# Kernel optimization log

Hardware: AMD Instinct MI355X
Metric: run time of the kernel (lower is better)

The kernel has to match this reference:

```python
import jax, jax.numpy as jnp
import numpy as np

EMBED_DIM = 1024
NUM_HEADS = 16
HEAD_DIM = EMBED_DIM // NUM_HEADS
WINDOW = 64


def apply_rope(x):
    # x: (B, H, S, d), rotate-half RoPE with base 10000
    B, H, S, d = x.shape
    half = d // 2
    pos = jnp.arange(S, dtype=x.dtype)
    freqs = 1.0 / (10000.0 ** (jnp.arange(half, dtype=x.dtype) / half))
    ang = pos[:, None] * freqs[None, :]              # (S, half)
    cos, sin = jnp.cos(ang), jnp.sin(ang)
    x1, x2 = x[..., :half], x[..., half:]
    return jnp.concatenate([x1 * cos - x2 * sin, x1 * sin + x2 * cos], axis=-1)


def setup_inputs() -> dict:
    key = jax.random.key(0)
    ks = jax.random.split(key, 12)
    B, S, D = 1, 2048, EMBED_DIM
    scale = 1.0 / np.sqrt(D)
    inp = {
        'query': jax.random.normal(ks[0], (B, S, D), jnp.float32),
        'key':   jax.random.normal(ks[1], (B, S, D), jnp.float32),
        'value': jax.random.normal(ks[2], (B, S, D), jnp.float32),
        'q_w': jax.random.normal(ks[3], (D, D), jnp.float32) * scale,
        'q_b': jax.random.normal(ks[4], (D,), jnp.float32) * 0.01,
        'k_w': jax.random.normal(ks[5], (D, D), jnp.float32) * scale,
        'k_b': jax.random.normal(ks[6], (D,), jnp.float32) * 0.01,
        'v_w': jax.random.normal(ks[7], (D, D), jnp.float32) * scale,
        'v_b': jax.random.normal(ks[8], (D,), jnp.float32) * 0.01,
        'o_w': jax.random.normal(ks[9], (D, D), jnp.float32) * scale,
        'o_b': jax.random.normal(ks[10], (D,), jnp.float32) * 0.01,
    }
    return inp


def _forward(query, key, value, q_w, q_b, k_w, k_b, v_w, v_b, o_w, o_b):
    B, S_q, D = query.shape
    S_k = key.shape[1]
    H, d, W = NUM_HEADS, HEAD_DIM, WINDOW

    q = (query @ q_w.T + q_b).reshape(B, S_q, H, d).transpose(0, 2, 1, 3)
    k = (key   @ k_w.T + k_b).reshape(B, S_k, H, d).transpose(0, 2, 1, 3)
    v = (value @ v_w.T + v_b).reshape(B, S_k, H, d).transpose(0, 2, 1, 3)

    q = apply_rope(q) * (d ** -0.5)
    k = apply_rope(k)

    # window indices: for query i, kv positions i-W .. i (invalid -> masked)
    q_pos = jnp.arange(S_q)[:, None]
    offsets = jnp.arange(-W, 1)[None, :]
    idx = q_pos + offsets                       # (S_q, W+1)
    local_mask = (idx < 0) | (idx >= S_k)       # (S_q, W+1)
    gidx = jnp.clip(idx, 0, S_k - 1)

    k_win = k[:, :, gidx, :]                    # (B, H, S_q, W+1, d)
    v_win = v[:, :, gidx, :]

    scores = jnp.einsum('bhqd,bhqwd->bhqw', q, k_win)
    mask = local_mask[None, None, :, :]
    scores = jnp.where(mask, -jnp.inf, scores)

    # safe softmax: fully-masked rows produce zeros
    m = jnp.max(scores, axis=-1, keepdims=True)
    m = jnp.where(jnp.isfinite(m), m, 0.0)
    e = jnp.exp(scores - m)
    denom = jnp.sum(e, axis=-1, keepdims=True)
    probs = jnp.where(denom > 0, e / jnp.where(denom > 0, denom, 1.0), 0.0)

    ctx = jnp.einsum('bhqw,bhqwd->bhqd', probs, v_win)
    ctx = ctx.transpose(0, 2, 1, 3).reshape(B, S_q, D)
    return ctx @ o_w.T + o_b


def reference(query, key, value, q_w, q_b, k_w, k_b, v_w, v_b, o_w, o_b):
    return _forward(query, key, value, q_w, q_b, k_w, k_b, v_w, v_b, o_w, o_b)
```

## Files before the change

kernel.cpp:

```cpp
#include <hip/hip_runtime.h>
#include <hip/hip_bf16.h>
#include <cstdint>
#include <cstddef>

typedef __attribute__((ext_vector_type(8))) short short8;
typedef __attribute__((ext_vector_type(4))) float f32x4;

__device__ __forceinline__ unsigned short f2bf(float f) {
  union { float f; uint32_t u; } c; c.f = f;
  uint32_t u = c.u;
  u += 0x7fffu + ((u >> 16) & 1u);
  return (unsigned short)(u >> 16);
}

__device__ __forceinline__ uint32_t pk_bf2(float lo, float hi) {
  return (uint32_t)f2bf(lo) | ((uint32_t)f2bf(hi) << 16);
}

__device__ __forceinline__ void gload16(const void* g, void* l) {
  __builtin_amdgcn_global_load_lds(
      (const __attribute__((address_space(1))) uint32_t*)g,
      (__attribute__((address_space(3))) uint32_t*)l, 16, 0, 0);
}

__global__ __launch_bounds__(512) void qkv_gemm(
    const float* __restrict__ Aq, const float* __restrict__ Ak,
    const float* __restrict__ Av,
    const float* __restrict__ Wq, const float* __restrict__ Wk,
    const float* __restrict__ Wv,
    const float* __restrict__ bq, const float* __restrict__ bk,
    const float* __restrict__ bv,
    unsigned short* __restrict__ Oq, unsigned short* __restrict__ Ok,
    unsigned short* __restrict__ OvT) {
  __shared__ __align__(16) unsigned short As[2][128][32];
  __shared__ __align__(16) unsigned short Bs[2][128][32];
  const int tid = threadIdx.x;
  const int w = tid >> 6, l = tid & 63;
  const int which = blockIdx.x >> 3;
  const int n0 = (blockIdx.x & 7) * 128;
  const int m0 = blockIdx.y * 128;
  const float* A = which == 0 ? Aq : which == 1 ? Ak : Av;
  const float* W = which == 0 ? Wq : which == 1 ? Wk : Wv;

  f32x4 acc[2][4];
#pragma unroll
  for (int a = 0; a < 2; ++a)
#pragma unroll
    for (int b = 0; b < 4; ++b) acc[a][b] = (f32x4){0.f, 0.f, 0.f, 0.f};

  const int wm = w >> 1, wn = w & 1;
  const int lr = l & 15, kq = l >> 4;
  const int srow = tid >> 2;
  const int scol = (tid & 3) * 8;

  float4 ra0, ra1, rw0, rw1;
  auto gload = [&](int kt) {
    const float* pa = A + (size_t)(m0 + srow) * 1024 + kt * 32 + scol;
    ra0 = *reinterpret_cast<const float4*>(pa);
    ra1 = *reinterpret_cast<const float4*>(pa + 4);
    const float* pw = W + (size_t)(n0 + srow) * 1024 + kt * 32 + scol;
    rw0 = *reinterpret_cast<const float4*>(pw);
    rw1 = *reinterpret_cast<const float4*>(pw + 4);
  };
  auto lwrite = [&](int b) {
    uint4 va = make_uint4(pk_bf2(ra0.x, ra0.y), pk_bf2(ra0.z, ra0.w),
                          pk_bf2(ra1.x, ra1.y), pk_bf2(ra1.z, ra1.w));
    uint4 vw = make_uint4(pk_bf2(rw0.x, rw0.y), pk_bf2(rw0.z, rw0.w),
                          pk_bf2(rw1.x, rw1.y), pk_bf2(rw1.z, rw1.w));
    *reinterpret_cast<uint4*>(&As[b][srow][scol]) = va;
    *reinterpret_cast<uint4*>(&Bs[b][srow][scol]) = vw;
  };

  gload(0);
  lwrite(0);
  __syncthreads();

  for (int kt = 0; kt < 32; ++kt) {
    const int cur = kt & 1;
    if (kt < 31) gload(kt + 1);
    short8 af[2], bf[4];
#pragma unroll
    for (int f = 0; f < 2; ++f)
      af[f] = *reinterpret_cast<const short8*>(&As[cur][wm * 32 + f * 16 + lr][kq * 8]);
#pragma unroll
    for (int f = 0; f < 4; ++f)
      bf[f] = *reinterpret_cast<const short8*>(&Bs[cur][wn * 64 + f * 16 + lr][kq * 8]);
#pragma unroll
    for (int fm = 0; fm < 2; ++fm)
#pragma unroll
      for (int fn = 0; fn < 4; ++fn)
        acc[fm][fn] = __builtin_amdgcn_mfma_f32_16x16x32_bf16(af[fm], bf[fn], acc[fm][fn], 0, 0, 0);
    if (kt < 31) lwrite(cur ^ 1);
    __syncthreads();
  }

  const float* bias = which == 0 ? bq : which == 1 ? bk : bv;
  if (which < 2) {
    unsigned short* Out = which == 0 ? Oq : Ok;
    const float sc = which == 0 ? 0.125f : 1.0f;
#pragma unroll
    for (int fn = 0; fn < 2; ++fn) {
      const int c1 = n0 + wn * 64 + fn * 16 + lr;
      const int c2 = c1 + 32;
      const int t = fn * 16 + lr;
      const float freq = exp2f(-(float)t * 0.415241012f);
      const float b1 = bias[c1], b2 = bias[c2];
#pragma unroll
      for (int fm = 0; fm < 2; ++fm) {
        const int rbase = m0 + wm * 32 + fm * 16 + kq * 4;
#pragma unroll
        for (int j = 0; j < 4; ++j) {
          const int s = rbase + j;
          float sn, cs;
          __sincosf((float)s * freq, &sn, &cs);
          const float x1 = acc[fm][fn][j] + b1;
          const float x2 = acc[fm][fn + 2][j] + b2;
          Out[(size_t)s * 1024 + c1] = f2bf((x1 * cs - x2 * sn) * sc);
          Out[(size_t)s * 1024 + c2] = f2bf((x1 * sn + x2 * cs) * sc);
        }
      }
    }
  } else {
#pragma unroll
    for (int fn = 0; fn < 4; ++fn) {
      const int c = n0 + wn * 64 + fn * 16 + lr;
      const float bb = bias[c];
#pragma unroll
      for (int fm = 0; fm < 2; ++fm) {
        const int rbase = m0 + wm * 32 + fm * 16 + kq * 4;
        ushort4 o;
        o.x = f2bf(acc[fm][fn][0] + bb);
        o.y = f2bf(acc[fm][fn][1] + bb);
        o.z = f2bf(acc[fm][fn][2] + bb);
        o.w = f2bf(acc[fm][fn][3] + bb);
        *reinterpret_cast<ushort4*>(OvT + (size_t)c * 2048 + rbase) = o;
      }
    }
  }
}

__global__ __launch_bounds__(256) void attn_kernel(
    const unsigned short* __restrict__ qr, const unsigned short* __restrict__ kr,
    const unsigned short* __restrict__ vT, unsigned short* __restrict__ ctx) {
  __shared__ __align__(16) unsigned short Ps[4][16][128];
  const int w = threadIdx.x >> 6, l = threadIdx.x & 63;
  const int h = blockIdx.x & 15, qb = blockIdx.x >> 4;
  const int i0 = qb * 64, hb = h * 64;
  const int r = l & 15, g = l >> 4;

  short8 qf[2];
#pragma unroll
  for (int kk = 0; kk < 2; ++kk)
    qf[kk] = *reinterpret_cast<const short8*>(
        qr + (size_t)(i0 + w * 16 + r) * 1024 + hb + kk * 32 + g * 8);

  f32x4 acc[8];
#pragma unroll
  for (int nt = 0; nt < 8; ++nt) acc[nt] = (f32x4){0.f, 0.f, 0.f, 0.f};
#pragma unroll
  for (int nt = 0; nt < 8; ++nt) {
    int kpos = i0 - 64 + nt * 16 + r;
    int krow = kpos < 0 ? 0 : kpos;
    const unsigned short* kp = kr + (size_t)krow * 1024 + hb + g * 8;
    short8 kf0 = *reinterpret_cast<const short8*>(kp);
    short8 kf1 = *reinterpret_cast<const short8*>(kp + 32);
    acc[nt] = __builtin_amdgcn_mfma_f32_16x16x32_bf16(qf[0], kf0, acc[nt], 0, 0, 0);
    acc[nt] = __builtin_amdgcn_mfma_f32_16x16x32_bf16(qf[1], kf1, acc[nt], 0, 0, 0);
  }

#pragma unroll
  for (int j = 0; j < 4; ++j) {
    const int iq = w * 16 + g * 4 + j;
    float sv[8];
    float m = -1e30f;
#pragma unroll
    for (int nt = 0; nt < 8; ++nt) {
      const int rel = nt * 16 + r - iq;
      const int kpos = i0 - 64 + nt * 16 + r;
      const bool ok = (rel >= 0) && (rel <= 64) && (kpos >= 0);
      sv[nt] = ok ? acc[nt][j] : -1e30f;
      m = fmaxf(m, sv[nt]);
    }
#pragma unroll
    for (int off = 8; off; off >>= 1) m = fmaxf(m, __shfl_xor(m, off));
    float e[8], den = 0.f;
#pragma unroll
    for (int nt = 0; nt < 8; ++nt) { e[nt] = __expf(sv[nt] - m); den += e[nt]; }
#pragma unroll
    for (int off = 8; off; off >>= 1) den += __shfl_xor(den, off);
    const float inv = 1.f / den;
    const int qrow = g * 4 + j;
    const int sw = (qrow & 7) << 3;
#pragma unroll
    for (int nt = 0; nt < 8; ++nt)
      Ps[w][qrow][(nt * 16 + r) ^ sw] = f2bf(e[nt] * inv);
  }

  __syncthreads();

  short8 pf[4];
  const int swr = (r & 7) << 3;
#pragma unroll
  for (int kk = 0; kk < 4; ++kk)
    pf[kk] = *reinterpret_cast<const short8*>(&Ps[w][r][(kk * 32 + g * 8) ^ swr]);

  f32x4 co[4];
#pragma unroll
  for (int n = 0; n < 4; ++n) co[n] = (f32x4){0.f, 0.f, 0.f, 0.f};
#pragma unroll
  for (int kk = 0; kk < 4; ++kk) {
    int cb = i0 - 64 + kk * 32 + g * 8;
    if (cb < 0) cb = 0;
#pragma unroll
    for (int n = 0; n < 4; ++n) {
      short8 vf = *reinterpret_cast<const short8*>(
          vT + (size_t)(hb + n * 16 + r) * 2048 + cb);
      co[n] = __builtin_amdgcn_mfma_f32_16x16x32_bf16(pf[kk], vf, co[n], 0, 0, 0);
    }
  }

#pragma unroll
  for (int n = 0; n < 4; ++n)
#pragma unroll
    for (int j = 0; j < 4; ++j)
      ctx[(size_t)(i0 + w * 16 + g * 4 + j) * 1024 + hb + n * 16 + r] = f2bf(co[n][j]);
}

__global__ __launch_bounds__(512) void oproj_gemm(
    const unsigned short* __restrict__ A, const float* __restrict__ W,
    const float* __restrict__ bias, float* __restrict__ Out) {
  __shared__ __align__(16) unsigned short As[2][128][32];
  __shared__ __align__(16) unsigned short Bs[2][64][32];
  const int tid = threadIdx.x;
  const int w = tid >> 6, l = tid & 63;
  const int n0 = blockIdx.x * 64;
  const int m0 = blockIdx.y * 128;

  f32x4 acc[2][2];
#pragma unroll
  for (int a = 0; a < 2; ++a)
#pragma unroll
    for (int b = 0; b < 2; ++b) acc[a][b] = (f32x4){0.f, 0.f, 0.f, 0.f};

  const int wm = w >> 1, wn = w & 1;
  const int lr = l & 15, kq = l >> 4;
  const int srow = tid >> 2;
  const int scol = (tid & 3) * 8;
  const int wrow = tid >> 3;
  const int wcol = (tid & 7) * 4;

  float4 rw;
  auto stageA = [&](int b, int kt) {
    gload16(A + (size_t)(m0 + srow) * 1024 + kt * 32 + scol,
            (char*)&As[b][0][0] + tid * 16);
  };
  auto gloadW = [&](int kt) {
    rw = *reinterpret_cast<const float4*>(W + (size_t)(n0 + wrow) * 1024 + kt * 32 + wcol);
  };
  auto lwriteW = [&](int b) {
    uint2 vw = make_uint2(pk_bf2(rw.x, rw.y), pk_bf2(rw.z, rw.w));
    *reinterpret_cast<uint2*>(&Bs[b][wrow][wcol]) = vw;
  };

  stageA(0, 0);
  gloadW(0);
  lwriteW(0);
  __syncthreads();

  for (int kt = 0; kt < 32; ++kt) {
    const int cur = kt & 1;
    if (kt < 31) { stageA(cur ^ 1, kt + 1); gloadW(kt + 1); }
    short8 af[2], bf[2];
#pragma unroll
    for (int f = 0; f < 2; ++f)
      af[f] = *reinterpret_cast<const short8*>(&As[cur][wm * 32 + f * 16 + lr][kq * 8]);
#pragma unroll
    for (int f = 0; f < 2; ++f)
      bf[f] = *reinterpret_cast<const short8*>(&Bs[cur][wn * 32 + f * 16 + lr][kq * 8]);
#pragma unroll
    for (int fm = 0; fm < 2; ++fm)
#pragma unroll
      for (int fn = 0; fn < 2; ++fn)
        acc[fm][fn] = __builtin_amdgcn_mfma_f32_16x16x32_bf16(af[fm], bf[fn], acc[fm][fn], 0, 0, 0);
    if (kt < 31) lwriteW(cur ^ 1);
    __syncthreads();
  }

#pragma unroll
  for (int fm = 0; fm < 2; ++fm) {
    const int rbase = m0 + wm * 32 + fm * 16 + kq * 4;
#pragma unroll
    for (int fn = 0; fn < 2; ++fn) {
      const int c = n0 + wn * 32 + fn * 16 + lr;
      const float bb = bias[c];
#pragma unroll
      for (int j = 0; j < 4; ++j)
        Out[(size_t)(rbase + j) * 1024 + c] = acc[fm][fn][j] + bb;
    }
  }
}

extern "C" void kernel_launch(void* const* d_in, const int* in_sizes, int n_in,
                              void* d_out, int out_size, void* d_ws, size_t ws_size,
                              hipStream_t stream) {
  const float* query = (const float*)d_in[0];
  const float* key   = (const float*)d_in[1];
  const float* value = (const float*)d_in[2];
  const float* q_w = (const float*)d_in[3];
  const float* q_b = (const float*)d_in[4];
  const float* k_w = (const float*)d_in[5];
  const float* k_b = (const float*)d_in[6];
  const float* v_w = (const float*)d_in[7];
  const float* v_b = (const float*)d_in[8];
  const float* o_w = (const float*)d_in[9];
  const float* o_b = (const float*)d_in[10];
  float* out = (float*)d_out;

  unsigned short* ws = (unsigned short*)d_ws;
  unsigned short* qrope = ws;
  unsigned short* krope = qrope + 2097152;
  unsigned short* vTb   = krope + 2097152;
  unsigned short* ctxb  = vTb + 2097152;

  qkv_gemm<<<dim3(24, 16), 512, 0, stream>>>(query, key, value, q_w, k_w, v_w,
                                             q_b, k_b, v_b, qrope, krope, vTb);
  attn_kernel<<<512, 256, 0, stream>>>(qrope, krope, vTb, ctxb);
  oproj_gemm<<<dim3(16, 16), 512, 0, stream>>>(ctxb, o_w, o_b, out);
}
```

Baseline: 78.35 us.

## Pad QKV GEMM LDS tiles, swizzle block order, deepen global prefetch

Pads the shared-memory A/B tiles from 32 to 40 shorts per row to reduce LDS bank conflicts on the MFMA fragment reads. Remaps the flat block index with a swizzle so that blocks running together are spread across Q/K/V and tiles, aiming for better L2 reuse. Restructures the K loop to keep two register stages of global loads in flight (prefetch distance two), hiding more global latency. This costs more registers and slightly more LDS, and it assumes the launch grid is exactly 24x16.

Result: no change. 77.75 us (-0.8%).

```diff
diff --git a/kernel.cpp b/kernel.cpp
--- a/kernel.cpp
+++ b/kernel.cpp
@@ -32,13 +32,18 @@
     const float* __restrict__ bv,
     unsigned short* __restrict__ Oq, unsigned short* __restrict__ Ok,
     unsigned short* __restrict__ OvT) {
-  __shared__ __align__(16) unsigned short As[2][128][32];
-  __shared__ __align__(16) unsigned short Bs[2][128][32];
+  __shared__ __align__(16) unsigned short As[2][128][40];
+  __shared__ __align__(16) unsigned short Bs[2][128][40];
   const int tid = threadIdx.x;
   const int w = tid >> 6, l = tid & 63;
-  const int which = blockIdx.x >> 3;
-  const int n0 = (blockIdx.x & 7) * 128;
-  const int m0 = blockIdx.y * 128;
+
+  const int flat = blockIdx.y * 24 + blockIdx.x;
+  const int swz = (flat & 7) * 48 + (flat >> 3);
+  const int which = swz >> 7;
+  const int rem = swz & 127;
+  const int m0 = (rem >> 3) * 128;
+  const int n0 = (rem & 7) * 128;
+
   const float* A = which == 0 ? Aq : which == 1 ? Ak : Av;
   const float* W = which == 0 ? Wq : which == 1 ? Wk : Wv;
 
@@ -53,31 +58,39 @@
   const int srow = tid >> 2;
   const int scol = (tid & 3) * 8;
 
-  float4 ra0, ra1, rw0, rw1;
-  auto gload = [&](int kt) {
-    const float* pa = A + (size_t)(m0 + srow) * 1024 + kt * 32 + scol;
-    ra0 = *reinterpret_cast<const float4*>(pa);
-    ra1 = *reinterpret_cast<const float4*>(pa + 4);
-    const float* pw = W + (size_t)(n0 + srow) * 1024 + kt * 32 + scol;
-    rw0 = *reinterpret_cast<const float4*>(pw);
-    rw1 = *reinterpret_cast<const float4*>(pw + 4);
-  };
-  auto lwrite = [&](int b) {
-    uint4 va = make_uint4(pk_bf2(ra0.x, ra0.y), pk_bf2(ra0.z, ra0.w),
-                          pk_bf2(ra1.x, ra1.y), pk_bf2(ra1.z, ra1.w));
-    uint4 vw = make_uint4(pk_bf2(rw0.x, rw0.y), pk_bf2(rw0.z, rw0.w),
-                          pk_bf2(rw1.x, rw1.y), pk_bf2(rw1.z, rw1.w));
-    *reinterpret_cast<uint4*>(&As[b][srow][scol]) = va;
-    *reinterpret_cast<uint4*>(&Bs[b][srow][scol]) = vw;
-  };
-
-  gload(0);
-  lwrite(0);
-  __syncthreads();
-
-  for (int kt = 0; kt < 32; ++kt) {
-    const int cur = kt & 1;
-    if (kt < 31) gload(kt + 1);
+  const float* pa = A + (size_t)(m0 + srow) * 1024 + scol;
+  const float* pw = W + (size_t)(n0 + srow) * 1024 + scol;
+
+  float4 a0A, a1A, w0A, w1A, a0B, a1B, w0B, w1B;
+  auto gloadA = [&](int kt) {
+    a0A = *reinterpret_cast<const float4*>(pa + kt * 32);
+    a1A = *reinterpret_cast<const float4*>(pa + kt * 32 + 4);
+    w0A = *reinterpret_cast<const float4*>(pw + kt * 32);
+    w1A = *reinterpret_cast<const float4*>(pw + kt * 32 + 4);
+  };
+  auto gloadB = [&](int kt) {
+    a0B = *reinterpret_cast<const float4*>(pa + kt * 32);
+    a1B = *reinterpret_cast<const float4*>(pa + kt * 32 + 4);
+    w0B = *reinterpret_cast<const float4*>(pw + kt * 32);
+    w1B = *reinterpret_cast<const float4*>(pw + kt * 32 + 4);
+  };
+  auto lwriteA = [&](int b) {
+    *reinterpret_cast<uint4*>(&As[b][srow][scol]) =
+        make_uint4(pk_bf2(a0A.x, a0A.y), pk_bf2(a0A.z, a0A.w),
+                   pk_bf2(a1A.x, a1A.y), pk_bf2(a1A.z, a1A.w));
+    *reinterpret_cast<uint4*>(&Bs[b][srow][scol]) =
+        make_uint4(pk_bf2(w0A.x, w0A.y), pk_bf2(w0A.z, w0A.w),
+                   pk_bf2(w1A.x, w1A.y), pk_bf2(w1A.z, w1A.w));
+  };
+  auto lwriteB = [&](int b) {
+    *reinterpret_cast<uint4*>(&As[b][srow][scol]) =
+        make_uint4(pk_bf2(a0B.x, a0B.y), pk_bf2(a0B.z, a0B.w),
+                   pk_bf2(a1B.x, a1B.y), pk_bf2(a1B.z, a1B.w));
+    *reinterpret_cast<uint4*>(&Bs[b][srow][scol]) =
+        make_uint4(pk_bf2(w0B.x, w0B.y), pk_bf2(w0B.z, w0B.w),
+                   pk_bf2(w1B.x, w1B.y), pk_bf2(w1B.z, w1B.w));
+  };
+  auto compute = [&](int cur) {
     short8 af[2], bf[4];
 #pragma unroll
     for (int f = 0; f < 2; ++f)
@@ -90,7 +103,22 @@
 #pragma unroll
       for (int fn = 0; fn < 4; ++fn)
         acc[fm][fn] = __builtin_amdgcn_mfma_f32_16x16x32_bf16(af[fm], bf[fn], acc[fm][fn], 0, 0, 0);
-    if (kt < 31) lwrite(cur ^ 1);
+  };
+
+  gloadA(0);
+  lwriteA(0);
+  gloadA(1);
+  __syncthreads();
+
+  for (int kt = 0; kt < 32; kt += 2) {
+    if (kt + 2 < 32) gloadB(kt + 2);
+    compute(0);
+    lwriteA(1);
+    __syncthreads();
+
+    if (kt + 3 < 32) gloadA(kt + 3);
+    compute(1);
+    if (kt + 2 < 32) lwriteB(0);
     __syncthreads();
   }
 
```
